# Kernel optimization log

Hardware: AMD Instinct MI355X
Metric: run time of the kernel (lower is better)

Reference implementation:

```python
import jax, jax.numpy as jnp
import numpy as np

B, T, C_FEAT, H = 1024, 256, 512, 256


def setup_inputs() -> dict:
    key = jax.random.key(0)
    ks = jax.random.split(key, 8)
    s_ih = 1.0 / np.sqrt(H)
    return {
        "features": jax.random.normal(ks[0], (B, T, C_FEAT), dtype=jnp.float32),
        "last_coord": jax.random.normal(ks[1], (B, 2), dtype=jnp.float32),
        "W_ih": jax.random.uniform(ks[2], (3 * H, C_FEAT + 2), jnp.float32, -s_ih, s_ih),
        "W_hh": jax.random.uniform(ks[3], (3 * H, H), jnp.float32, -s_ih, s_ih),
        "b_ih": jax.random.uniform(ks[4], (3 * H,), jnp.float32, -s_ih, s_ih),
        "b_hh": jax.random.uniform(ks[5], (3 * H,), jnp.float32, -s_ih, s_ih),
        "W_proj": jax.random.uniform(ks[6], (2, H), jnp.float32, -s_ih, s_ih),
        "b_proj": jax.random.uniform(ks[7], (2,), jnp.float32, -s_ih, s_ih),
    }


def reference(features, last_coord, W_ih, W_hh, b_ih, b_hh, W_proj, b_proj):
    # features: (B, T, C_feat); last_coord: (B, 2)
    Bb, Tt, Cf = features.shape
    Hh = W_hh.shape[1]
    h0 = jnp.zeros((Bb, Hh), dtype=features.dtype)

    def step(carry, feat_t):
        h, coord = carry
        x = jnp.concatenate([feat_t, coord], axis=1)          # (B, C+2)
        gi = x @ W_ih.T + b_ih                                 # (B, 3H)
        gh = h @ W_hh.T + b_hh                                 # (B, 3H)
        i_r, i_z, i_n = jnp.split(gi, 3, axis=1)
        h_r, h_z, h_n = jnp.split(gh, 3, axis=1)
        r = jax.nn.sigmoid(i_r + h_r)
        z = jax.nn.sigmoid(i_z + h_z)
        n = jnp.tanh(i_n + r * h_n)
        h_new = (1.0 - z) * n + z * h                          # PyTorch GRU update
        disp = h_new @ W_proj.T + b_proj                       # (B, 2)
        return (h_new, coord + disp), disp

    feats_t = jnp.swapaxes(features, 0, 1)                     # (T, B, C)
    _, disps = jax.lax.scan(step, (h0, last_coord), feats_t)   # (T, B, 2)
    return jnp.swapaxes(disps, 0, 1)                           # (B, T, 2)
```

## Files before the change

kernel.cpp:

```cpp
#include <hip/hip_runtime.h>
#include <stdint.h>

typedef unsigned short u16;
typedef unsigned int   u32;
typedef __attribute__((ext_vector_type(8))) __bf16 bf16x8;
typedef __attribute__((ext_vector_type(4))) float  f32x4;
typedef __attribute__((ext_vector_type(8))) u16    u16x8;
typedef __attribute__((ext_vector_type(4))) u16    u16x4;
typedef __attribute__((ext_vector_type(2))) u32    u32x2;

__device__ __forceinline__ u16 f2bf(float f) {
    u32 u = __float_as_uint(f);
    u32 r = (u + 0x7fffu + ((u >> 16) & 1u)) >> 16;
    return (u16)r;
}
__device__ __forceinline__ float bf2f(u16 v) { return __uint_as_float(((u32)v) << 16); }
__device__ __forceinline__ bf16x8 as_bf(u16x8 x) { union { u16x8 a; bf16x8 b; } u; u.a = x; return u.b; }
__device__ __forceinline__ void gload_lds16(const void* g, void* l) {
    __builtin_amdgcn_global_load_lds((const __attribute__((address_space(1))) void*)g,
                                     (__attribute__((address_space(3))) void*)l, 16, 0, 0);
}

__global__ void k_prep(const float* __restrict__ W_ih, const float* __restrict__ W_hh,
                       const float* __restrict__ b_ih, const float* __restrict__ b_hh,
                       u16* __restrict__ Wf, u16* __restrict__ Whh, float* __restrict__ bsum) {
    int i = blockIdx.x * 256 + threadIdx.x;
    if (i < 768 * 512) { int o = i >> 9, k = i & 511; Wf[i] = f2bf(W_ih[o * 514 + k]); }
    if (i < 768 * 256) { Whh[i] = f2bf(W_hh[i]); }
    if (i < 768)       { bsum[i] = b_ih[i] + (i < 512 ? b_hh[i] : 0.f); }
}

__global__ void k_cast(const float* __restrict__ f, u16* __restrict__ o) {
    const size_t N8 = (size_t)262144 * 512 / 8;
    for (size_t i = (size_t)blockIdx.x * 256 + threadIdx.x; i < N8; i += (size_t)gridDim.x * 256) {
        float4 a = ((const float4*)f)[i * 2];
        float4 b = ((const float4*)f)[i * 2 + 1];
        u16x8 v;
        v[0] = f2bf(a.x); v[1] = f2bf(a.y); v[2] = f2bf(a.z); v[3] = f2bf(a.w);
        v[4] = f2bf(b.x); v[5] = f2bf(b.y); v[6] = f2bf(b.z); v[7] = f2bf(b.w);
        ((u16x8*)o)[i] = v;
    }
}

__device__ __forceinline__ void xcd_remap(int& n0, int& m0) {
    int phys = blockIdx.x + blockIdx.y * 6;
    int logical = (phys & 7) * 1536 + (phys >> 3);
    n0 = (logical % 6) * 128;
    m0 = (logical / 6) * 128;
}

__global__ __launch_bounds__(256) void k_gemm(const u16* __restrict__ featbf,
                                              const u16* __restrict__ Wf,
                                              const float* __restrict__ bsum,
                                              float* __restrict__ Gf) {
    __shared__ u16 As[128 * 64];
    __shared__ u16 Bs[128 * 64];
    const int tid = threadIdx.x;
    const int l = tid & 63, wv = tid >> 6;
    const int wr = wv >> 1, wc = wv & 1;
    const int lb = l & 15, lq = l >> 4;
    int n0, m0; xcd_remap(n0, m0);
    const int rl = l >> 3;
    const int c16 = (l & 7) * 16;
    const int sswz = (rl & 7) << 4;

    f32x4 acc[4][4] = {};

    for (int k0 = 0; k0 < 512; k0 += 64) {
        __syncthreads();
#pragma unroll
        for (int i = 0; i < 4; ++i) {
            int ci = wv * 4 + i;
            int r = ci * 8 + rl;
            const char* sa = (const char*)(featbf + (size_t)(m0 + r) * 512) + k0 * 2 + (c16 ^ sswz);
            gload_lds16(sa, (char*)As + ci * 1024);
            const char* sb = (const char*)(Wf + (size_t)(n0 + r) * 512) + k0 * 2 + (c16 ^ sswz);
            gload_lds16(sb, (char*)Bs + ci * 1024);
        }
        __syncthreads();
#pragma unroll
        for (int kc = 0; kc < 2; ++kc) {
            bf16x8 af[4], bfr[4];
#pragma unroll
            for (int mi = 0; mi < 4; ++mi) {
                int row = wr * 64 + mi * 16 + lb;
                af[mi] = *(const bf16x8*)((char*)As + row * 128 + (((kc * 32 + lq * 8) * 2) ^ ((row & 7) << 4)));
            }
#pragma unroll
            for (int ni = 0; ni < 4; ++ni) {
                int row = wc * 64 + ni * 16 + lb;
                bfr[ni] = *(const bf16x8*)((char*)Bs + row * 128 + (((kc * 32 + lq * 8) * 2) ^ ((row & 7) << 4)));
            }
#pragma unroll
            for (int mi = 0; mi < 4; ++mi)
#pragma unroll
                for (int ni = 0; ni < 4; ++ni)
                    acc[mi][ni] = __builtin_amdgcn_mfma_f32_16x16x32_bf16(af[mi], bfr[ni], acc[mi][ni], 0, 0, 0);
        }
    }
#pragma unroll
    for (int ni = 0; ni < 4; ++ni) {
        int o = n0 + wc * 64 + ni * 16 + lb;
        float bi = bsum[o];
#pragma unroll
        for (int mi = 0; mi < 4; ++mi) {
#pragma unroll
            for (int j = 0; j < 4; ++j) {
                int m = m0 + wr * 64 + mi * 16 + lq * 4 + j;
                int bb = m >> 8, tt = m & 255;
                Gf[(size_t)((tt << 10) + bb) * 768 + o] = acc[mi][ni][j] + bi;
            }
        }
    }
}

template<typename ST>
__global__ __launch_bounds__(256) void k_gemm_legacy(const float* __restrict__ feat,
                                                     const u16* __restrict__ Wf,
                                                     const float* __restrict__ bsum,
                                                     ST* __restrict__ Gf) {
    __shared__ u16 As[128 * 64];
    __shared__ u16 Bs[128 * 64];
    const int tid = threadIdx.x;
    const int l = tid & 63, wv = tid >> 6;
    const int wr = wv >> 1, wc = wv & 1;
    const int lb = l & 15, lq = l >> 4;
    int n0, m0; xcd_remap(n0, m0);
    const int srow = tid >> 1, scol = (tid & 1) * 32;

    f32x4 acc[4][4] = {};

    for (int k0 = 0; k0 < 512; k0 += 64) {
        __syncthreads();
        const float* ga = feat + (size_t)(m0 + srow) * 512 + k0 + scol;
        const u16*   gb = Wf + (n0 + srow) * 512 + k0 + scol;
        char* arow = (char*)As + srow * 128;
        char* brow = (char*)Bs + srow * 128;
        const int swz = (srow & 7) << 4;
#pragma unroll
        for (int i = 0; i < 4; ++i) {
            float4 f0 = *(const float4*)(ga + i * 8);
            float4 f1 = *(const float4*)(ga + i * 8 + 4);
            u16x8 v;
            v[0] = f2bf(f0.x); v[1] = f2bf(f0.y); v[2] = f2bf(f0.z); v[3] = f2bf(f0.w);
            v[4] = f2bf(f1.x); v[5] = f2bf(f1.y); v[6] = f2bf(f1.z); v[7] = f2bf(f1.w);
            *(u16x8*)(arow + (((scol + i * 8) * 2) ^ swz)) = v;
            u16x8 w8 = *(const u16x8*)(gb + i * 8);
            *(u16x8*)(brow + (((scol + i * 8) * 2) ^ swz)) = w8;
        }
        __syncthreads();
#pragma unroll
        for (int kc = 0; kc < 2; ++kc) {
            bf16x8 af[4], bfr[4];
#pragma unroll
            for (int mi = 0; mi < 4; ++mi) {
                int row = wr * 64 + mi * 16 + lb;
                af[mi] = *(const bf16x8*)((char*)As + row * 128 + (((kc * 32 + lq * 8) * 2) ^ ((row & 7) << 4)));
            }
#pragma unroll
            for (int ni = 0; ni < 4; ++ni) {
                int row = wc * 64 + ni * 16 + lb;
                bfr[ni] = *(const bf16x8*)((char*)Bs + row * 128 + (((kc * 32 + lq * 8) * 2) ^ ((row & 7) << 4)));
            }
#pragma unroll
            for (int mi = 0; mi < 4; ++mi)
#pragma unroll
                for (int ni = 0; ni < 4; ++ni)
                    acc[mi][ni] = __builtin_amdgcn_mfma_f32_16x16x32_bf16(af[mi], bfr[ni], acc[mi][ni], 0, 0, 0);
        }
    }
#pragma unroll
    for (int ni = 0; ni < 4; ++ni) {
        int o = n0 + wc * 64 + ni * 16 + lb;
        float bi = bsum[o];
#pragma unroll
        for (int mi = 0; mi < 4; ++mi) {
#pragma unroll
            for (int j = 0; j < 4; ++j) {
                int m = m0 + wr * 64 + mi * 16 + lq * 4 + j;
                int bb = m >> 8, tt = m & 255;
                size_t idx = (size_t)((tt << 10) + bb) * 768 + o;
                float v = acc[mi][ni][j] + bi;
                if constexpr (sizeof(ST) == 4) Gf[idx] = v; else Gf[idx] = f2bf(v);
            }
        }
    }
}

template<typename ST>
__global__ __launch_bounds__(512, 2) void k_rnn(const float* __restrict__ lastc,
                                                const float* __restrict__ W_ih,
                                                const float* __restrict__ bhh_g,
                                                const float* __restrict__ Wp,
                                                const float* __restrict__ bp,
                                                const u16* __restrict__ Whh,
                                                const ST* __restrict__ Gf,
                                                float* __restrict__ out) {
    __shared__ u16 Wlds[96 * 512];
    __shared__ u16 hbf[2][16 * 320];
    __shared__ float wpL[256 * 2];
    __shared__ float coordL[16 * 2];
    __shared__ float dPart[8 * 16 * 2];

    const int tid = threadIdx.x, l = tid & 63, wv = tid >> 6;
    const int lb = l & 15, lq = l >> 4;
    const int bb = blockIdx.x << 4;
    const int swz = (lb & 7) << 4;

    bf16x8 wres[6][3][2];
    bf16x8 wcf[3][2];
    float bhhn[2][4];
#pragma unroll
    for (int g = 0; g < 3; ++g)
#pragma unroll
        for (int ut = 0; ut < 2; ++ut) {
            int row = g * 256 + (2 * wv + ut) * 16 + lb;
#pragma unroll
            for (int kc = 0; kc < 6; ++kc)
                wres[kc][g][ut] = *(const bf16x8*)(Whh + row * 256 + kc * 32 + lq * 8);
            u16x8 cf = {0, 0, 0, 0, 0, 0, 0, 0};
            if (lq == 0) {
                cf[0] = f2bf(W_ih[row * 514 + 512]);
                cf[1] = f2bf(W_ih[row * 514 + 513]);
            }
            wcf[g][ut] = as_bf(cf);
        }
#pragma unroll
    for (int ut = 0; ut < 2; ++ut)
#pragma unroll
        for (int j = 0; j < 4; ++j)
            bhhn[ut][j] = bhh_g[512 + (2 * wv + ut) * 16 + lq * 4 + j];

    for (int i = tid; i < 24576; i += 512) {
        int s = i >> 8, r = i & 255, ll = r >> 2, e = r & 3;
        int g = s >> 5, rem = s & 31, tt = rem >> 1, kcs = rem & 1;
        int row = g * 256 + tt * 16 + (ll & 15);
        int k = (6 + kcs) * 32 + (ll >> 4) * 8 + e * 2;
        ((u32*)Wlds)[i] = *(const u32*)(Whh + row * 256 + k);
    }
    for (int i = tid; i < 2 * 16 * 320 / 2; i += 512) ((u32*)hbf)[i] = 0u;
    if (tid < 256) { wpL[tid * 2] = Wp[tid]; wpL[tid * 2 + 1] = Wp[256 + tid]; }
    float bpc = (tid < 32) ? bp[tid & 1] : 0.f;
    __syncthreads();
    if (tid < 32) {
        int b = tid >> 1, c = tid & 1;
        float cc = lastc[(bb + b) * 2 + c];
        coordL[b * 2 + c] = cc;
        *(u16*)((char*)hbf + b * 640 + 512 + ((c * 2) ^ ((b & 7) << 4))) = f2bf(cc);
    }
    __syncthreads();

    float hreg[2][4] = {};
    const ST* gr = Gf + (size_t)(bb + lb) * 768 + lq * 4;
    int par = 0;

    for (int t = 0; t < 256; ++t) {
        float gf[3][2][4];
#pragma unroll
        for (int g = 0; g < 3; ++g)
#pragma unroll
            for (int ut = 0; ut < 2; ++ut) {
                int off = g * 256 + (2 * wv + ut) * 16;
                if constexpr (sizeof(ST) == 4) {
                    float4 v = *(const float4*)(gr + off);
                    gf[g][ut][0] = v.x; gf[g][ut][1] = v.y; gf[g][ut][2] = v.z; gf[g][ut][3] = v.w;
                } else {
                    u16x4 v = *(const u16x4*)(gr + off);
#pragma unroll
                    for (int j = 0; j < 4; ++j) gf[g][ut][j] = bf2f(v[j]);
                }
            }

        const char* hrow = (const char*)hbf + par * 10240 + lb * 640;
        f32x4 acc[3][2] = {};
        f32x4 accC[2] = {};
#pragma unroll
        for (int kc = 0; kc < 6; ++kc) {
            bf16x8 hb = *(const bf16x8*)(hrow + ((kc * 64 + lq * 16) ^ swz));
#pragma unroll
            for (int g = 0; g < 3; ++g)
#pragma unroll
                for (int ut = 0; ut < 2; ++ut)
                    acc[g][ut] = __builtin_amdgcn_mfma_f32_16x16x32_bf16(wres[kc][g][ut], hb, acc[g][ut], 0, 0, 0);
        }
#pragma unroll
        for (int kcs = 0; kcs < 2; ++kcs) {
            bf16x8 hb = *(const bf16x8*)(hrow + (((6 + kcs) * 64 + lq * 16) ^ swz));
#pragma unroll
            for (int g = 0; g < 3; ++g)
#pragma unroll
                for (int ut = 0; ut < 2; ++ut) {
                    int s = (g * 16 + (2 * wv + ut)) * 2 + kcs;
                    bf16x8 wl = *(const bf16x8*)((const char*)Wlds + s * 1024 + l * 16);
                    acc[g][ut] = __builtin_amdgcn_mfma_f32_16x16x32_bf16(wl, hb, acc[g][ut], 0, 0, 0);
                }
        }
        {
            bf16x8 hbE = *(const bf16x8*)(hrow + 512 + ((lq * 16) ^ swz));
#pragma unroll
            for (int ut = 0; ut < 2; ++ut) {
                acc[0][ut] = __builtin_amdgcn_mfma_f32_16x16x32_bf16(wcf[0][ut], hbE, acc[0][ut], 0, 0, 0);
                acc[1][ut] = __builtin_amdgcn_mfma_f32_16x16x32_bf16(wcf[1][ut], hbE, acc[1][ut], 0, 0, 0);
                accC[ut]   = __builtin_amdgcn_mfma_f32_16x16x32_bf16(wcf[2][ut], hbE, accC[ut],   0, 0, 0);
            }
        }

        char* hwr = (char*)hbf + (par ^ 1) * 10240 + lb * 640;
        float pd0 = 0.f, pd1 = 0.f;
#pragma unroll
        for (int ut = 0; ut < 2; ++ut) {
            int ub = (2 * wv + ut) * 16 + lq * 4;
            float4 wpa = *(const float4*)(wpL + ub * 2);
            float4 wpb = *(const float4*)(wpL + ub * 2 + 4);
            u16 hpk[4];
#pragma unroll
            for (int j = 0; j < 4; ++j) {
                float r = 1.f / (1.f + __expf(-(gf[0][ut][j] + acc[0][ut][j])));
                float z = 1.f / (1.f + __expf(-(gf[1][ut][j] + acc[1][ut][j])));
                float ghn = acc[2][ut][j] + bhhn[ut][j];
                float xn = gf[2][ut][j] + accC[ut][j] + r * ghn;
                float e = __expf(-2.f * fabsf(xn));
                float th = (1.f - e) / (1.f + e);
                th = (xn >= 0.f) ? th : -th;
                float hn = (1.f - z) * th + z * hreg[ut][j];
                hreg[ut][j] = hn;
                float w0 = (j == 0) ? wpa.x : (j == 1) ? wpa.z : (j == 2) ? wpb.x : wpb.z;
                float w1 = (j == 0) ? wpa.y : (j == 1) ? wpa.w : (j == 2) ? wpb.y : wpb.w;
                pd0 += w0 * hn;
                pd1 += w1 * hn;
                hpk[j] = f2bf(hn);
            }
            u32x2 pv;
            pv.x = (u32)hpk[0] | ((u32)hpk[1] << 16);
            pv.y = (u32)hpk[2] | ((u32)hpk[3] << 16);
            *(u32x2*)(hwr + ((ub * 2) ^ swz)) = pv;
        }
        pd0 += __shfl_xor(pd0, 16); pd0 += __shfl_xor(pd0, 32);
        pd1 += __shfl_xor(pd1, 16); pd1 += __shfl_xor(pd1, 32);
        if (l < 16) { dPart[(wv * 16 + l) * 2] = pd0; dPart[(wv * 16 + l) * 2 + 1] = pd1; }
        __syncthreads();

        if (tid < 32) {
            int b = tid >> 1, c = tid & 1;
            float d = bpc;
#pragma unroll
            for (int w8 = 0; w8 < 8; ++w8) d += dPart[(w8 * 16 + b) * 2 + c];
            out[((size_t)(bb + b) * 256 + t) * 2 + c] = d;
            float nc = coordL[b * 2 + c] + d;
            coordL[b * 2 + c] = nc;
            *(u16*)((char*)hbf + (par ^ 1) * 10240 + b * 640 + 512 + ((c * 2) ^ ((b & 7) << 4))) = f2bf(nc);
        }
        __syncthreads();
        par ^= 1;
        gr += (size_t)1024 * 768;
    }
}

extern "C" void kernel_launch(void* const* d_in, const int* in_sizes, int n_in,
                              void* d_out, int out_size, void* d_ws, size_t ws_size,
                              hipStream_t stream) {
    const float* feat   = (const float*)d_in[0];
    const float* lastc  = (const float*)d_in[1];
    const float* W_ih   = (const float*)d_in[2];
    const float* W_hh   = (const float*)d_in[3];
    const float* b_ih   = (const float*)d_in[4];
    const float* b_hh   = (const float*)d_in[5];
    const float* W_proj = (const float*)d_in[6];
    const float* b_proj = (const float*)d_in[7];
    float* out = (float*)d_out;

    char* ws = (char*)d_ws;
    u16*   Wf    = (u16*)ws;
    u16*   Whh   = (u16*)(ws + 786432);
    float* bsum  = (float*)(ws + 786432 + 393216);
    const size_t off_fb = 786432 + 393216 + 3072;
    u16*   featbf = (u16*)(ws + off_fb);
    const size_t off_gf_full = off_fb + (size_t)262144 * 512 * 2;
    const size_t need_full  = off_gf_full + (size_t)262144 * 768 * 4;
    const size_t need_tier2 = off_fb + (size_t)262144 * 768 * 4;

    k_prep<<<1536, 256, 0, stream>>>(W_ih, W_hh, b_ih, b_hh, Wf, Whh, bsum);

    if (ws_size >= need_full) {
        float* Gf = (float*)(ws + off_gf_full);
        k_cast<<<16384, 256, 0, stream>>>(feat, featbf);
        k_gemm<<<dim3(6, 2048), 256, 0, stream>>>(featbf, Wf, bsum, Gf);
        k_rnn<float><<<64, 512, 0, stream>>>(lastc, W_ih, b_hh, W_proj, b_proj, Whh, Gf, out);
    } else if (ws_size >= need_tier2) {
        float* Gf = (float*)(ws + off_fb);
        k_gemm_legacy<float><<<dim3(6, 2048), 256, 0, stream>>>(feat, Wf, bsum, Gf);
        k_rnn<float><<<64, 512, 0, stream>>>(lastc, W_ih, b_hh, W_proj, b_proj, Whh, Gf, out);
    } else {
        u16* Gf = (u16*)(ws + off_fb);
        k_gemm_legacy<u16><<<dim3(6, 2048), 256, 0, stream>>>(feat, Wf, bsum, Gf);
        k_rnn<u16><<<64, 512, 0, stream>>>(lastc, W_ih, b_hh, W_proj, b_proj, Whh, Gf, out);
    }
}
```

Before: 1.531 ms.

## Apply coordinate input weights in fp32 per thread instead of via extra MFMA

The coordinate contribution to the GRU input gates was previously handled by bf16 MFMAs on an extra padded h column. It is now computed in fp32 on each thread from W_ih coordinate columns held in LDS. Every thread also reduces the projection partials itself and keeps its own copy of the coordinates, which removes the serial tid<32 stage and the coordL state. Output stores are deferred by one step so they leave the critical path. This cuts six MFMAs and some synchronised serial work per timestep, and raises coordinate precision, at the cost of extra LDS reads and VALU work per thread.

After: 1.603 ms. 4.7% more time.

```diff
diff --git a/kernel.cpp b/kernel.cpp
--- a/kernel.cpp
+++ b/kernel.cpp
@@ -8,6 +8,7 @@
 typedef __attribute__((ext_vector_type(8))) u16    u16x8;
 typedef __attribute__((ext_vector_type(4))) u16    u16x4;
 typedef __attribute__((ext_vector_type(2))) u32    u32x2;
+typedef __attribute__((ext_vector_type(2))) float  f32x2;
 
 __device__ __forceinline__ u16 f2bf(float f) {
     u32 u = __float_as_uint(f);
@@ -15,7 +16,6 @@
     return (u16)r;
 }
 __device__ __forceinline__ float bf2f(u16 v) { return __uint_as_float(((u32)v) << 16); }
-__device__ __forceinline__ bf16x8 as_bf(u16x8 x) { union { u16x8 a; bf16x8 b; } u; u.a = x; return u.b; }
 __device__ __forceinline__ void gload_lds16(const void* g, void* l) {
     __builtin_amdgcn_global_load_lds((const __attribute__((address_space(1))) void*)g,
                                      (__attribute__((address_space(3))) void*)l, 16, 0, 0);
@@ -197,10 +197,10 @@
                                                 const ST* __restrict__ Gf,
                                                 float* __restrict__ out) {
     __shared__ u16 Wlds[96 * 512];
-    __shared__ u16 hbf[2][16 * 320];
+    __shared__ u16 hbf[2][16 * 256];
+    __shared__ f32x2 wcxyL[768];
     __shared__ float wpL[256 * 2];
-    __shared__ float coordL[16 * 2];
-    __shared__ float dPart[8 * 16 * 2];
+    __shared__ float dPart[16][2][8];
 
     const int tid = threadIdx.x, l = tid & 63, wv = tid >> 6;
     const int lb = l & 15, lq = l >> 4;
@@ -208,7 +208,6 @@
     const int swz = (lb & 7) << 4;
 
     bf16x8 wres[6][3][2];
-    bf16x8 wcf[3][2];
     float bhhn[2][4];
 #pragma unroll
     for (int g = 0; g < 3; ++g)
@@ -218,12 +217,6 @@
 #pragma unroll
             for (int kc = 0; kc < 6; ++kc)
                 wres[kc][g][ut] = *(const bf16x8*)(Whh + row * 256 + kc * 32 + lq * 8);
-            u16x8 cf = {0, 0, 0, 0, 0, 0, 0, 0};
-            if (lq == 0) {
-                cf[0] = f2bf(W_ih[row * 514 + 512]);
-                cf[1] = f2bf(W_ih[row * 514 + 513]);
-            }
-            wcf[g][ut] = as_bf(cf);
         }
 #pragma unroll
     for (int ut = 0; ut < 2; ++ut)
@@ -238,23 +231,27 @@
         int k = (6 + kcs) * 32 + (ll >> 4) * 8 + e * 2;
         ((u32*)Wlds)[i] = *(const u32*)(Whh + row * 256 + k);
     }
-    for (int i = tid; i < 2 * 16 * 320 / 2; i += 512) ((u32*)hbf)[i] = 0u;
+    for (int i = tid; i < 2 * 16 * 256 / 2; i += 512) ((u32*)hbf)[i] = 0u;
+    for (int i = tid; i < 768; i += 512) {
+        f32x2 w; w.x = W_ih[i * 514 + 512]; w.y = W_ih[i * 514 + 513];
+        wcxyL[i] = w;
+    }
     if (tid < 256) { wpL[tid * 2] = Wp[tid]; wpL[tid * 2 + 1] = Wp[256 + tid]; }
-    float bpc = (tid < 32) ? bp[tid & 1] : 0.f;
+    const float bp0 = bp[0], bp1 = bp[1];
+    float cx = lastc[(bb + lb) * 2], cy = lastc[(bb + lb) * 2 + 1];
     __syncthreads();
-    if (tid < 32) {
-        int b = tid >> 1, c = tid & 1;
-        float cc = lastc[(bb + b) * 2 + c];
-        coordL[b * 2 + c] = cc;
-        *(u16*)((char*)hbf + b * 640 + 512 + ((c * 2) ^ ((b & 7) << 4))) = f2bf(cc);
-    }
-    __syncthreads();
 
     float hreg[2][4] = {};
+    float prevD0 = 0.f, prevD1 = 0.f;
     const ST* gr = Gf + (size_t)(bb + lb) * 768 + lq * 4;
     int par = 0;
 
     for (int t = 0; t < 256; ++t) {
+        if (t > 0 && wv == 0 && lq == 0) {
+            f32x2 d; d.x = prevD0; d.y = prevD1;
+            *(f32x2*)(out + ((size_t)(bb + lb) * 256 + (t - 1)) * 2) = d;
+        }
+
         float gf[3][2][4];
 #pragma unroll
         for (int g = 0; g < 3; ++g)
@@ -271,9 +268,8 @@
                 }
             }
 
-        const char* hrow = (const char*)hbf + par * 10240 + lb * 640;
+        const char* hrow = (const char*)hbf + par * 8192 + lb * 512;
         f32x4 acc[3][2] = {};
-        f32x4 accC[2] = {};
 #pragma unroll
         for (int kc = 0; kc < 6; ++kc) {
             bf16x8 hb = *(const bf16x8*)(hrow + ((kc * 64 + lq * 16) ^ swz));
@@ -295,30 +291,34 @@
                     acc[g][ut] = __builtin_amdgcn_mfma_f32_16x16x32_bf16(wl, hb, acc[g][ut], 0, 0, 0);
                 }
         }
-        {
-            bf16x8 hbE = *(const bf16x8*)(hrow + 512 + ((lq * 16) ^ swz));
-#pragma unroll
-            for (int ut = 0; ut < 2; ++ut) {
-                acc[0][ut] = __builtin_amdgcn_mfma_f32_16x16x32_bf16(wcf[0][ut], hbE, acc[0][ut], 0, 0, 0);
-                acc[1][ut] = __builtin_amdgcn_mfma_f32_16x16x32_bf16(wcf[1][ut], hbE, acc[1][ut], 0, 0, 0);
-                accC[ut]   = __builtin_amdgcn_mfma_f32_16x16x32_bf16(wcf[2][ut], hbE, accC[ut],   0, 0, 0);
-            }
-        }
-
-        char* hwr = (char*)hbf + (par ^ 1) * 10240 + lb * 640;
+
+        char* hwr = (char*)hbf + (par ^ 1) * 8192 + lb * 512;
         float pd0 = 0.f, pd1 = 0.f;
 #pragma unroll
         for (int ut = 0; ut < 2; ++ut) {
-            int ub = (2 * wv + ut) * 16 + lq * 4;
+            int row0 = (2 * wv + ut) * 16 + lq * 4;
+            int ub = row0;
             float4 wpa = *(const float4*)(wpL + ub * 2);
             float4 wpb = *(const float4*)(wpL + ub * 2 + 4);
+            float4 cr0 = *(const float4*)(&wcxyL[row0]);
+            float4 cr1 = *(const float4*)(&wcxyL[row0 + 2]);
+            float4 cz0 = *(const float4*)(&wcxyL[256 + row0]);
+            float4 cz1 = *(const float4*)(&wcxyL[256 + row0 + 2]);
+            float4 cn0 = *(const float4*)(&wcxyL[512 + row0]);
+            float4 cn1 = *(const float4*)(&wcxyL[512 + row0 + 2]);
+            float ctr[4] = { cr0.x * cx + cr0.y * cy, cr0.z * cx + cr0.w * cy,
+                             cr1.x * cx + cr1.y * cy, cr1.z * cx + cr1.w * cy };
+            float ctz[4] = { cz0.x * cx + cz0.y * cy, cz0.z * cx + cz0.w * cy,
+                             cz1.x * cx + cz1.y * cy, cz1.z * cx + cz1.w * cy };
+            float ctn[4] = { cn0.x * cx + cn0.y * cy, cn0.z * cx + cn0.w * cy,
+                             cn1.x * cx + cn1.y * cy, cn1.z * cx + cn1.w * cy };
             u16 hpk[4];
 #pragma unroll
             for (int j = 0; j < 4; ++j) {
-                float r = 1.f / (1.f + __expf(-(gf[0][ut][j] + acc[0][ut][j])));
-                float z = 1.f / (1.f + __expf(-(gf[1][ut][j] + acc[1][ut][j])));
+                float r = 1.f / (1.f + __expf(-(gf[0][ut][j] + ctr[j] + acc[0][ut][j])));
+                float z = 1.f / (1.f + __expf(-(gf[1][ut][j] + ctz[j] + acc[1][ut][j])));
                 float ghn = acc[2][ut][j] + bhhn[ut][j];
-                float xn = gf[2][ut][j] + accC[ut][j] + r * ghn;
+                float xn = gf[2][ut][j] + ctn[j] + r * ghn;
                 float e = __expf(-2.f * fabsf(xn));
                 float th = (1.f - e) / (1.f + e);
                 th = (xn >= 0.f) ? th : -th;
@@ -337,22 +337,26 @@
         }
         pd0 += __shfl_xor(pd0, 16); pd0 += __shfl_xor(pd0, 32);
         pd1 += __shfl_xor(pd1, 16); pd1 += __shfl_xor(pd1, 32);
-        if (l < 16) { dPart[(wv * 16 + l) * 2] = pd0; dPart[(wv * 16 + l) * 2 + 1] = pd1; }
-        __syncthreads();
-
-        if (tid < 32) {
-            int b = tid >> 1, c = tid & 1;
-            float d = bpc;
-#pragma unroll
-            for (int w8 = 0; w8 < 8; ++w8) d += dPart[(w8 * 16 + b) * 2 + c];
-            out[((size_t)(bb + b) * 256 + t) * 2 + c] = d;
-            float nc = coordL[b * 2 + c] + d;
-            coordL[b * 2 + c] = nc;
-            *(u16*)((char*)hbf + (par ^ 1) * 10240 + b * 640 + 512 + ((c * 2) ^ ((b & 7) << 4))) = f2bf(nc);
+        if (l < 16) { dPart[l][0][wv] = pd0; dPart[l][1][wv] = pd1; }
+        __syncthreads();
+
+        {
+            float4 a0 = *(const float4*)(&dPart[lb][0][0]);
+            float4 a1 = *(const float4*)(&dPart[lb][0][4]);
+            float4 b0 = *(const float4*)(&dPart[lb][1][0]);
+            float4 b1 = *(const float4*)(&dPart[lb][1][4]);
+            float d0 = bp0 + a0.x + a0.y + a0.z + a0.w + a1.x + a1.y + a1.z + a1.w;
+            float d1 = bp1 + b0.x + b0.y + b0.z + b0.w + b1.x + b1.y + b1.z + b1.w;
+            cx += d0; cy += d1;
+            prevD0 = d0; prevD1 = d1;
         }
         __syncthreads();
         par ^= 1;
         gr += (size_t)1024 * 768;
+    }
+    if (wv == 0 && lq == 0) {
+        f32x2 d; d.x = prevD0; d.y = prevD1;
+        *(f32x2*)(out + ((size_t)(bb + lb) * 256 + 255) * 2) = d;
     }
 }
 
```
